# Performance work log

Hardware: AMD Instinct MI355X
Metric: run time of the kernel (lower is better)

## Reference

```python
import jax, jax.numpy as jnp
import numpy as np

NUM_HEADS = 4
HID = 64
NUM_LAYERS = 3
NEG_SLOPE = 0.2  # PyG GATConv default


def setup_inputs() -> dict:
    key = jax.random.key(0)
    ks = jax.random.split(key, 6)
    B, N, D = 64, 512, 64
    return {
        "embeddings": jax.random.normal(ks[0], (B, N, D), jnp.float32),
        "lin_w": jax.random.normal(ks[1], (NUM_LAYERS, NUM_HEADS * HID, D), jnp.float32) * 0.1,
        "att_src": jax.random.normal(ks[2], (NUM_LAYERS, NUM_HEADS, HID), jnp.float32) * 0.1,
        "att_dst": jax.random.normal(ks[3], (NUM_LAYERS, NUM_HEADS, HID), jnp.float32) * 0.1,
        "conv_b": jnp.zeros((NUM_LAYERS, HID), jnp.float32),
        "readout_w": jax.random.normal(ks[4], (D, HID), jnp.float32) * 0.1,
        "readout_b": jnp.zeros((D,), jnp.float32),
    }


def reference(embeddings, lin_w, att_src, att_dst, conv_b, readout_w, readout_b):
    # Graph is fully connected (combinations + reversed) and PyG GATConv adds
    # self-loops by default -> attention softmax over ALL nodes j for each i.
    B, N, _ = embeddings.shape
    x = embeddings
    for l in range(NUM_LAYERS):
        h = jnp.einsum('bnd,od->bno', x, lin_w[l]).reshape(B, N, NUM_HEADS, HID)  # [B,N,H,C]
        a_src = jnp.einsum('bnhc,hc->bnh', h, att_src[l])  # per source node j
        a_dst = jnp.einsum('bnhc,hc->bnh', h, att_dst[l])  # per target node i
        e = a_dst[:, :, None, :] + a_src[:, None, :, :]    # [B,i,j,H]
        e = jnp.where(e >= 0, e, NEG_SLOPE * e)            # LeakyReLU(0.2)
        alpha = jax.nn.softmax(e, axis=2)                  # softmax over neighbors j
        out = jnp.einsum('bijh,bjhc->bihc', alpha, h).mean(axis=2) + conv_b[l]  # concat=False -> head mean
        x = jax.nn.relu(out)
    pooled = x.mean(axis=1)                                # mean over nodes
    return pooled @ readout_w.T + readout_b                # [B, D]
```

## Files before the change

### kernel.cpp

```cpp
#include <hip/hip_runtime.h>
#include <math.h>


using short8  = __attribute__((ext_vector_type(8))) short;
using floatx4 = __attribute__((ext_vector_type(4))) float;

__device__ inline unsigned short f2bf(float f) {
    union { float f; unsigned u; } v; v.f = f;
    unsigned u = v.u + 0x7FFFu + ((v.u >> 16) & 1u);
    return (unsigned short)(u >> 16);
}
__device__ inline float bf2f(unsigned short s) {
    union { float f; unsigned u; } v; v.u = ((unsigned)s) << 16;
    return v.f;
}

__device__ inline void cvt8(const float4 a, const float4 b, short8& hi, short8& lo) {
    float f[8] = {a.x, a.y, a.z, a.w, b.x, b.y, b.z, b.w};
    short8 H, L;
#pragma unroll
    for (int i = 0; i < 8; ++i) {
        unsigned short h = f2bf(f[i]);
        H[i] = (short)h;
        L[i] = (short)f2bf(f[i] - bf2f(h));
    }
    hi = H; lo = L;
}

__global__ __launch_bounds__(512) void linprep_kernel(const float* __restrict__ x,
                                                      const float* __restrict__ W,
                                                      const float* __restrict__ att_src,
                                                      const float* __restrict__ att_dst,
                                                      float* __restrict__ hT,
                                                      float4* __restrict__ g_rE,
                                                      float4* __restrict__ g_abk) {
    __shared__ unsigned short WH[64 * 72], WL[64 * 72];
    __shared__ float sA[512], dA[512];
    __shared__ int   s_idxE[512];
    __shared__ float z1suf[513], z2pre[513];
    __shared__ float wred[8];

    const int t  = threadIdx.x;
    const int r8 = blockIdx.x & 7;
    const int q  = blockIdx.x >> 3;
    const int ct = q & 3;
    const int b  = ((q >> 2) << 3) | r8;
    const int bh = b * 4 + ct;
    const int c0 = ct * 64;

#pragma unroll
    for (int qq = 0; qq < 2; ++qq) {
        int f = qq * 512 + t;
        int wrow = f >> 4, d4 = f & 15;
        float4 v = *(const float4*)(W + (size_t)(c0 + wrow) * 64 + d4 * 4);
        unsigned short h0 = f2bf(v.x), h1 = f2bf(v.y), h2 = f2bf(v.z), h3 = f2bf(v.w);
        ushort4 hi = make_ushort4(h0, h1, h2, h3);
        ushort4 lo = make_ushort4(f2bf(v.x - bf2f(h0)), f2bf(v.y - bf2f(h1)),
                                  f2bf(v.z - bf2f(h2)), f2bf(v.w - bf2f(h3)));
        *(ushort4*)&WH[wrow * 72 + d4 * 4] = hi;
        *(ushort4*)&WL[wrow * 72 + d4 * 4] = lo;
    }
    __syncthreads();

    const int lane = t & 63, wv = t >> 6;
    const int mrow = lane & 15, quad = lane >> 4;

    short8 bhf[4][2], blf[4][2];
#pragma unroll
    for (int g = 0; g < 4; ++g)
#pragma unroll
        for (int kk = 0; kk < 2; ++kk) {
            int ko = kk * 32 + quad * 8;
            bhf[g][kk] = *(const short8*)&WH[(g * 16 + mrow) * 72 + ko];
            blf[g][kk] = *(const short8*)&WL[(g * 16 + mrow) * 72 + ko];
        }
    float as_g[4], ad_g[4];
#pragma unroll
    for (int g = 0; g < 4; ++g) {
        as_g[g] = att_src[c0 + g * 16 + mrow];
        ad_g[g] = att_dst[c0 + g * 16 + mrow];
    }

    const float* xbase = x + (size_t)(b * 512 + mrow) * 64 + quad * 8;
    float4 nxa = *(const float4*)(xbase + (size_t)wv * 1024);
    float4 nxb = *(const float4*)(xbase + (size_t)wv * 1024 + 4);
    float4 nxc = *(const float4*)(xbase + (size_t)wv * 1024 + 32);
    float4 nxd = *(const float4*)(xbase + (size_t)wv * 1024 + 36);

#pragma unroll 1
    for (int tl = wv; tl < 32; tl += 8) {
        float4 xa = nxa, xb = nxb, xc = nxc, xd = nxd;
        if (tl + 8 < 32) {
            const float* nb = xbase + (size_t)(tl + 8) * 1024;
            nxa = *(const float4*)(nb);
            nxb = *(const float4*)(nb + 4);
            nxc = *(const float4*)(nb + 32);
            nxd = *(const float4*)(nb + 36);
        }
        short8 ah0, al0, ah1, al1;
        cvt8(xa, xb, ah0, al0);
        cvt8(xc, xd, ah1, al1);

        floatx4 acc[4];
#pragma unroll
        for (int g = 0; g < 4; ++g) {
            floatx4 a = {0.f, 0.f, 0.f, 0.f};
            a = __builtin_amdgcn_mfma_f32_16x16x32_bf16(ah0, bhf[g][0], a, 0, 0, 0);
            a = __builtin_amdgcn_mfma_f32_16x16x32_bf16(ah1, bhf[g][1], a, 0, 0, 0);
            a = __builtin_amdgcn_mfma_f32_16x16x32_bf16(ah0, blf[g][0], a, 0, 0, 0);
            a = __builtin_amdgcn_mfma_f32_16x16x32_bf16(ah1, blf[g][1], a, 0, 0, 0);
            a = __builtin_amdgcn_mfma_f32_16x16x32_bf16(al0, bhf[g][0], a, 0, 0, 0);
            a = __builtin_amdgcn_mfma_f32_16x16x32_bf16(al1, bhf[g][1], a, 0, 0, 0);
            acc[g] = a;
        }

        const int nbase = b * 512 + tl * 16 + quad * 4;
#pragma unroll
        for (int g = 0; g < 4; ++g) {
            float tmp0 = __shfl_xor(acc[g][0], 1, 64);
            float tmp1 = __shfl_xor(acc[g][1], 1, 64);
            float tmp2 = __shfl_xor(acc[g][2], 1, 64);
            float tmp3 = __shfl_xor(acc[g][3], 1, 64);
            const size_t cp = (size_t)(ct * 32 + g * 8 + (mrow >> 1));
            if ((mrow & 1) == 0) {
                *(float4*)&hT[cp * 65536 + (size_t)nbase * 2] =
                    make_float4(acc[g][0], tmp0, acc[g][1], tmp1);
            } else {
                *(float4*)&hT[cp * 65536 + (size_t)(nbase + 2) * 2] =
                    make_float4(tmp2, acc[g][2], tmp3, acc[g][3]);
            }
        }

        float ps[4], pd[4];
#pragma unroll
        for (int reg = 0; reg < 4; ++reg) {
            ps[reg] = acc[0][reg] * as_g[0] + acc[1][reg] * as_g[1]
                    + acc[2][reg] * as_g[2] + acc[3][reg] * as_g[3];
            pd[reg] = acc[0][reg] * ad_g[0] + acc[1][reg] * ad_g[1]
                    + acc[2][reg] * ad_g[2] + acc[3][reg] * ad_g[3];
        }
#pragma unroll
        for (int m = 1; m <= 8; m <<= 1) {
#pragma unroll
            for (int reg = 0; reg < 4; ++reg) {
                ps[reg] += __shfl_xor(ps[reg], m, 64);
                pd[reg] += __shfl_xor(pd[reg], m, 64);
            }
        }
        if (mrow < 4) {
            sA[tl * 16 + quad * 4 + mrow] = ps[mrow];
            dA[tl * 16 + quad * 4 + mrow] = pd[mrow];
        }
    }
    __syncthreads();

    const bool act = (t < 256);
    const int wid = t >> 6;

    float dreg[2] = {0.f, 0.f};
    if (act) {
        dreg[0] = dA[t];
        dreg[1] = dA[t + 256];
    }

    float v0 = 0.f, v1 = 0.f;
    int id0 = 0, id1 = 0;
    if (act) { v0 = sA[2 * t]; v1 = sA[2 * t + 1]; id0 = 2 * t; id1 = 2 * t + 1; }

    for (int k = 2; k <= 512; k <<= 1) {
        for (int j = k >> 1; j >= 1; j >>= 1) {
            bool asc = ((t & (k >> 1)) == 0);
            if (j == 1) {
                if (act) {
                    bool sw = asc ? (v0 > v1) : (v0 < v1);
                    if (sw) { float tv = v0; v0 = v1; v1 = tv; int ti = id0; id0 = id1; id1 = ti; }
                }
            } else if (j <= 64) {
                if (act) {
                    int m = j >> 1;
                    float w0 = __shfl_xor(v0, m, 64);
                    int  wi0 = __shfl_xor(id0, m, 64);
                    float w1 = __shfl_xor(v1, m, 64);
                    int  wi1 = __shfl_xor(id1, m, 64);
                    bool low = ((t & m) == 0);
                    bool wantmin = (low == asc);
                    if (wantmin ? (w0 < v0) : (w0 > v0)) { v0 = w0; id0 = wi0; }
                    if (wantmin ? (w1 < v1) : (w1 > v1)) { v1 = w1; id1 = wi1; }
                }
            } else {
                int m = j >> 1;
                if (act) {
                    sA[2 * t] = v0; sA[2 * t + 1] = v1;
                    s_idxE[2 * t] = id0; s_idxE[2 * t + 1] = id1;
                }
                __syncthreads();
                if (act) {
                    int tp = t ^ m;
                    float w0 = sA[2 * tp], w1 = sA[2 * tp + 1];
                    int wi0 = s_idxE[2 * tp], wi1 = s_idxE[2 * tp + 1];
                    bool low = ((t & m) == 0);
                    bool wantmin = (low == asc);
                    if (wantmin ? (w0 < v0) : (w0 > v0)) { v0 = w0; id0 = wi0; }
                    if (wantmin ? (w1 < v1) : (w1 > v1)) { v1 = w1; id1 = wi1; }
                }
                __syncthreads();
            }
        }
    }

    if (act) { sA[2 * t] = v0; sA[2 * t + 1] = v1; }
    __syncthreads();
    const float M = sA[511];

    float e1_0 = 0.f, e1_1 = 0.f, e2_0 = 0.f, e2_1 = 0.f;
    if (act) {
        e1_0 = __expf(v0 - M);  e1_1 = __expf(v1 - M);
        e2_0 = __expf(0.2f * (v0 - M));  e2_1 = __expf(0.2f * (v1 - M));
        const int base = bh * 512;
        g_rE[base + id0] = make_float4(__int_as_float(2 * t),     e1_0, e2_0, 0.f);
        g_rE[base + id1] = make_float4(__int_as_float(2 * t + 1), e1_1, e2_1, 0.f);
    }

    float S1 = e1_0 + e1_1, S2 = e2_0 + e2_1;
    float i1 = S1, i2 = S2;
    if (act) {
        for (int off = 1; off < 64; off <<= 1) {
            float u1 = __shfl_up(i1, off, 64);
            float u2 = __shfl_up(i2, off, 64);
            if (lane >= off) { i1 += u1; i2 += u2; }
        }
        if (lane == 63) { wred[wid] = i1; wred[4 + wid] = i2; }
    }
    __syncthreads();
    if (act) {
        float off1 = 0.f, off2 = 0.f;
        for (int w = 0; w < wid; ++w) { off1 += wred[w]; off2 += wred[4 + w]; }
        const float T1 = wred[0] + wred[1] + wred[2] + wred[3];
        const float T2 = wred[4] + wred[5] + wred[6] + wred[7];
        float pre1 = off1 + i1 - S1;
        float pre2 = off2 + i2 - S2;
        z1suf[2 * t] = T1 - pre1;
        z1suf[2 * t + 1] = T1 - pre1 - e1_0;
        z2pre[2 * t] = pre2;
        z2pre[2 * t + 1] = pre2 + e2_0;
        if (t == 0) { z1suf[512] = 0.f; z2pre[512] = T2; }
    }
    __syncthreads();

    if (act) {
        for (int rr = 0; rr < 2; ++rr) {
            int i = t + rr * 256;
            float d = dreg[rr];
            int lo = 0, hi = 512;
            while (lo < hi) {
                int mid = (lo + hi) >> 1;
                if (d + sA[mid] >= 0.f) hi = mid; else lo = mid + 1;
            }
            int k = lo;
            float g = d + M;
            float G = (g >= 0.f) ? g : 0.2f * g;
            float al = __expf(g - G);
            float be = __expf(0.2f * g - G);
            float Z = al * z1suf[k] + be * z2pre[k];
            float inv = 1.0f / Z;
            g_abk[bh * 512 + i] = make_float4(al * inv, be * inv,
                                              __int_as_float(k), 0.f);
        }
    }
}

__global__ __launch_bounds__(256) void attn_agg_fin(const float* __restrict__ hT,
                                                    const float4* __restrict__ g_rE,
                                                    const float4* __restrict__ g_abk,
                                                    const float* __restrict__ bias,
                                                    float* __restrict__ x,
                                                    float* __restrict__ pooled,
                                                    int storex) {
    const int r8 = blockIdx.x & 7;
    const int qq = blockIdx.x >> 3;
    const int cg = qq & 31;
    const int b  = ((qq >> 5) << 3) | r8;
    const int c0 = cg * 2;
    const int t = threadIdx.x;
    const int lane = t & 63, wv = t >> 6;

    __shared__ float4 A12[4][512];
    __shared__ float tots[4][2];
    __shared__ float sredP[4][2];

    {
        const int bh = b * 4 + wv;
        const int base = bh * 512;
        const float* hTb = hT + (size_t)(wv * 32 + cg) * 65536 + (size_t)(b * 512) * 2;
#pragma unroll
        for (int it = 0; it < 8; ++it) {
            int j = it * 64 + lane;
            float4 rE = g_rE[base + j];
            int rk = __float_as_int(rE.x);
            float2 hv = *(const float2*)&hTb[j * 2];
            int pk = ((rk & 7) << 6) | (rk >> 3);
            A12[wv][pk] = make_float4(rE.y * hv.x, rE.z * hv.x,
                                      rE.y * hv.y, rE.z * hv.y);
        }
        float a1c0[8], a2c0[8], a1c1[8], a2c1[8];
#pragma unroll
        for (int i = 0; i < 8; ++i) {
            float4 vv = A12[wv][i * 64 + lane];
            a1c0[i] = vv.x; a2c0[i] = vv.y; a1c1[i] = vv.z; a2c1[i] = vv.w;
        }
        float s10 = 0.f, s20 = 0.f, s11 = 0.f, s21 = 0.f;
#pragma unroll
        for (int i = 0; i < 8; ++i) {
            s10 += a1c0[i]; s20 += a2c0[i]; s11 += a1c1[i]; s21 += a2c1[i];
        }
        float suf0 = s10, suf1 = s11;
#pragma unroll
        for (int off = 1; off < 64; off <<= 1) {
            float u0 = __shfl_down(suf0, off, 64);
            float u1 = __shfl_down(suf1, off, 64);
            if (lane + off < 64) { suf0 += u0; suf1 += u1; }
        }
        float run0 = suf0 - s10, run1 = suf1 - s11;
        float pre0 = s20, pre1 = s21;
#pragma unroll
        for (int off = 1; off < 64; off <<= 1) {
            float u0 = __shfl_up(pre0, off, 64);
            float u1 = __shfl_up(pre1, off, 64);
            if (lane >= off) { pre0 += u0; pre1 += u1; }
        }
        float run20 = pre0 - s20, run21 = pre1 - s21;
        if (lane == 63) { tots[wv][0] = pre0; tots[wv][1] = pre1; }
#pragma unroll
        for (int i = 7; i >= 0; --i) {
            run0 += a1c0[i]; a1c0[i] = run0;
            run1 += a1c1[i]; a1c1[i] = run1;
        }
#pragma unroll
        for (int i = 0; i < 8; ++i) {
            float tv0 = a2c0[i]; a2c0[i] = run20; run20 += tv0;
            float tv1 = a2c1[i]; a2c1[i] = run21; run21 += tv1;
        }
#pragma unroll
        for (int i = 0; i < 8; ++i)
            A12[wv][i * 64 + lane] = make_float4(a1c0[i], a2c0[i],
                                                 a1c1[i], a2c1[i]);
    }
    __syncthreads();

    const float bv0 = bias[c0], bv1 = bias[c0 + 1];
    float p0 = 0.f, p1 = 0.f;
#pragma unroll
    for (int rr = 0; rr < 2; ++rr) {
        const int i = t + rr * 256;
        float a0 = 0.f, a1 = 0.f;
#pragma unroll
        for (int head = 0; head < 4; ++head) {
            const int base = (b * 4 + head) * 512;
            float4 abk = g_abk[base + i];
            int k = __float_as_int(abk.z);
            if (k < 512) {
                int pk = ((k & 7) << 6) | (k >> 3);
                float4 vv = A12[head][pk];
                a0 += abk.x * vv.x + abk.y * vv.y;
                a1 += abk.x * vv.z + abk.y * vv.w;
            } else {
                a0 += abk.y * tots[head][0];
                a1 += abk.y * tots[head][1];
            }
        }
        float2 o = make_float2(fmaxf(0.25f * a0 + bv0, 0.f),
                               fmaxf(0.25f * a1 + bv1, 0.f));
        if (storex) *(float2*)&x[(size_t)(b * 512 + i) * 64 + c0] = o;
        p0 += o.x; p1 += o.y;
    }

#pragma unroll
    for (int m = 1; m <= 32; m <<= 1) {
        p0 += __shfl_xor(p0, m, 64);
        p1 += __shfl_xor(p1, m, 64);
    }
    if (lane == 0) { sredP[wv][0] = p0; sredP[wv][1] = p1; }
    __syncthreads();
    if (t == 0) {
        pooled[b * 64 + c0]     = sredP[0][0] + sredP[1][0] + sredP[2][0] + sredP[3][0];
        pooled[b * 64 + c0 + 1] = sredP[0][1] + sredP[1][1] + sredP[2][1] + sredP[3][1];
    }
}

__global__ __launch_bounds__(64) void readout_kernel(const float* __restrict__ pooled,
                                                     const float* __restrict__ rw,
                                                     const float* __restrict__ rb,
                                                     float* __restrict__ out) {
    __shared__ float pl[64];
    int b = blockIdx.x, t = threadIdx.x;
    pl[t] = pooled[b * 64 + t] * (1.0f / 512.0f);
    __syncthreads();
    float a = rb[t];
    for (int cc = 0; cc < 64; ++cc) a += pl[cc] * rw[t * 64 + cc];
    out[b * 64 + t] = a;
}

extern "C" void kernel_launch(void* const* d_in, const int* in_sizes, int n_in,
                              void* d_out, int out_size, void* d_ws, size_t ws_size,
                              hipStream_t stream) {
    const float* emb       = (const float*)d_in[0];
    const float* lin_w     = (const float*)d_in[1];
    const float* att_src   = (const float*)d_in[2];
    const float* att_dst   = (const float*)d_in[3];
    const float* conv_b    = (const float*)d_in[4];
    const float* readout_w = (const float*)d_in[5];
    const float* readout_b = (const float*)d_in[6];
    float* out = (float*)d_out;

    float* ws   = (float*)d_ws;
    float* xbuf = ws;
    float* hT   = ws + 2097152;
    float* meta = ws + 10485760;

    float4* g_rE   = (float4*)meta;
    float4* g_abk  = (float4*)(meta + 524288);
    float*  pooled = ws + 11534336;

    for (int l = 0; l < 3; ++l) {
        const float* xin = (l == 0) ? emb : xbuf;
        linprep_kernel<<<256, 512, 0, stream>>>(xin, lin_w + (size_t)l * 16384,
                                                att_src + l * 256, att_dst + l * 256,
                                                hT, g_rE, g_abk);
        attn_agg_fin<<<2048, 256, 0, stream>>>(hT, g_rE, g_abk,
                                               conv_b + l * 64, xbuf, pooled,
                                               (l < 2) ? 1 : 0);
    }
    readout_kernel<<<64, 64, 0, stream>>>(pooled, readout_w, readout_b, out);
}
```

Baseline: 196.4 us.

## Split fused linear+prep kernel into parallel GEMM and separate sort/prefix kernel

The fused linprep kernel ran 256 blocks of 512 threads, with half the threads idle during the sort and prefix phase. This splits it into a lin_kernel over 1024 blocks of 256 threads, where each block handles a quarter of the node tiles and writes src/dst attention scores to a global buffer. A new prep_kernel with 256 blocks of 256 threads then does the bitonic sort, prefix sums and per-row search. The aim is more parallelism and occupancy for the GEMM; the cost is an extra launch per layer, a global round-trip for the scores, and re-converting the weight tile to bf16 in four times as many blocks.

```diff
diff --git a/kernel.cpp b/kernel.cpp
--- a/kernel.cpp
+++ b/kernel.cpp
@@ -27,30 +27,27 @@
     hi = H; lo = L;
 }
 
-__global__ __launch_bounds__(512) void linprep_kernel(const float* __restrict__ x,
-                                                      const float* __restrict__ W,
-                                                      const float* __restrict__ att_src,
-                                                      const float* __restrict__ att_dst,
-                                                      float* __restrict__ hT,
-                                                      float4* __restrict__ g_rE,
-                                                      float4* __restrict__ g_abk) {
+__global__ __launch_bounds__(256) void lin_kernel(const float* __restrict__ x,
+                                                  const float* __restrict__ W,
+                                                  const float* __restrict__ att_src,
+                                                  const float* __restrict__ att_dst,
+                                                  float* __restrict__ hT,
+                                                  float2* __restrict__ g_sd) {
     __shared__ unsigned short WH[64 * 72], WL[64 * 72];
-    __shared__ float sA[512], dA[512];
-    __shared__ int   s_idxE[512];
-    __shared__ float z1suf[513], z2pre[513];
-    __shared__ float wred[8];
 
     const int t  = threadIdx.x;
-    const int r8 = blockIdx.x & 7;
-    const int q  = blockIdx.x >> 3;
-    const int ct = q & 3;
-    const int b  = ((q >> 2) << 3) | r8;
-    const int bh = b * 4 + ct;
-    const int c0 = ct * 64;
-
-#pragma unroll
-    for (int qq = 0; qq < 2; ++qq) {
-        int f = qq * 512 + t;
+    const int r8   = blockIdx.x & 7;
+    const int rest = blockIdx.x >> 3;
+    const int bhi  = rest >> 4;
+    const int ct   = (rest >> 2) & 3;
+    const int q4   = rest & 3;
+    const int b    = (bhi << 3) | r8;
+    const int bh   = b * 4 + ct;
+    const int c0   = ct * 64;
+
+#pragma unroll
+    for (int qq = 0; qq < 4; ++qq) {
+        int f = qq * 256 + t;
         int wrow = f >> 4, d4 = f & 15;
         float4 v = *(const float4*)(W + (size_t)(c0 + wrow) * 64 + d4 * 4);
         unsigned short h0 = f2bf(v.x), h1 = f2bf(v.y), h2 = f2bf(v.z), h3 = f2bf(v.w);
@@ -81,17 +78,19 @@
         ad_g[g] = att_dst[c0 + g * 16 + mrow];
     }
 
+    const int tl0 = q4 * 8 + wv;
     const float* xbase = x + (size_t)(b * 512 + mrow) * 64 + quad * 8;
-    float4 nxa = *(const float4*)(xbase + (size_t)wv * 1024);
-    float4 nxb = *(const float4*)(xbase + (size_t)wv * 1024 + 4);
-    float4 nxc = *(const float4*)(xbase + (size_t)wv * 1024 + 32);
-    float4 nxd = *(const float4*)(xbase + (size_t)wv * 1024 + 36);
+    float4 nxa = *(const float4*)(xbase + (size_t)tl0 * 1024);
+    float4 nxb = *(const float4*)(xbase + (size_t)tl0 * 1024 + 4);
+    float4 nxc = *(const float4*)(xbase + (size_t)tl0 * 1024 + 32);
+    float4 nxd = *(const float4*)(xbase + (size_t)tl0 * 1024 + 36);
 
 #pragma unroll 1
-    for (int tl = wv; tl < 32; tl += 8) {
+    for (int ii = 0; ii < 2; ++ii) {
+        const int tl = tl0 + ii * 4;
         float4 xa = nxa, xb = nxb, xc = nxc, xd = nxd;
-        if (tl + 8 < 32) {
-            const float* nb = xbase + (size_t)(tl + 8) * 1024;
+        if (ii == 0) {
+            const float* nb = xbase + (size_t)(tl + 4) * 1024;
             nxa = *(const float4*)(nb);
             nxb = *(const float4*)(nb + 4);
             nxc = *(const float4*)(nb + 32);
@@ -148,74 +147,76 @@
             }
         }
         if (mrow < 4) {
-            sA[tl * 16 + quad * 4 + mrow] = ps[mrow];
-            dA[tl * 16 + quad * 4 + mrow] = pd[mrow];
-        }
-    }
-    __syncthreads();
-
-    const bool act = (t < 256);
+            g_sd[bh * 512 + tl * 16 + quad * 4 + mrow] =
+                make_float2(ps[mrow], pd[mrow]);
+        }
+    }
+}
+
+__global__ __launch_bounds__(256) void prep_kernel(const float2* __restrict__ g_sd,
+                                                   float4* __restrict__ g_rE,
+                                                   float4* __restrict__ g_abk) {
+    __shared__ float sA[512], dA[512];
+    __shared__ int   s_idxE[512];
+    __shared__ float z1suf[513], z2pre[513];
+    __shared__ float wred[8];
+
+    const int bh = blockIdx.x;
+    const int t = threadIdx.x;
+    const int lane = t & 63;
     const int wid = t >> 6;
 
-    float dreg[2] = {0.f, 0.f};
-    if (act) {
-        dreg[0] = dA[t];
-        dreg[1] = dA[t + 256];
-    }
-
-    float v0 = 0.f, v1 = 0.f;
-    int id0 = 0, id1 = 0;
-    if (act) { v0 = sA[2 * t]; v1 = sA[2 * t + 1]; id0 = 2 * t; id1 = 2 * t + 1; }
-
+    for (int rr = 0; rr < 2; ++rr) {
+        int j = t + rr * 256;
+        float2 sd = g_sd[bh * 512 + j];
+        sA[j] = sd.x;
+        dA[j] = sd.y;
+    }
+    __syncthreads();
+
+    float dreg[2] = {dA[t], dA[t + 256]};
+
+    float v0 = sA[2 * t], v1 = sA[2 * t + 1];
+    int id0 = 2 * t, id1 = 2 * t + 1;
     for (int k = 2; k <= 512; k <<= 1) {
         for (int j = k >> 1; j >= 1; j >>= 1) {
             bool asc = ((t & (k >> 1)) == 0);
             if (j == 1) {
-                if (act) {
-                    bool sw = asc ? (v0 > v1) : (v0 < v1);
-                    if (sw) { float tv = v0; v0 = v1; v1 = tv; int ti = id0; id0 = id1; id1 = ti; }
-                }
+                bool sw = asc ? (v0 > v1) : (v0 < v1);
+                if (sw) { float tv = v0; v0 = v1; v1 = tv; int ti = id0; id0 = id1; id1 = ti; }
             } else if (j <= 64) {
-                if (act) {
-                    int m = j >> 1;
-                    float w0 = __shfl_xor(v0, m, 64);
-                    int  wi0 = __shfl_xor(id0, m, 64);
-                    float w1 = __shfl_xor(v1, m, 64);
-                    int  wi1 = __shfl_xor(id1, m, 64);
-                    bool low = ((t & m) == 0);
-                    bool wantmin = (low == asc);
-                    if (wantmin ? (w0 < v0) : (w0 > v0)) { v0 = w0; id0 = wi0; }
-                    if (wantmin ? (w1 < v1) : (w1 > v1)) { v1 = w1; id1 = wi1; }
-                }
+                int m = j >> 1;
+                float w0 = __shfl_xor(v0, m, 64);
+                int  wi0 = __shfl_xor(id0, m, 64);
+                float w1 = __shfl_xor(v1, m, 64);
+                int  wi1 = __shfl_xor(id1, m, 64);
+                bool low = ((t & m) == 0);
+                bool wantmin = (low == asc);
+                if (wantmin ? (w0 < v0) : (w0 > v0)) { v0 = w0; id0 = wi0; }
+                if (wantmin ? (w1 < v1) : (w1 > v1)) { v1 = w1; id1 = wi1; }
             } else {
                 int m = j >> 1;
-                if (act) {
-                    sA[2 * t] = v0; sA[2 * t + 1] = v1;
-                    s_idxE[2 * t] = id0; s_idxE[2 * t + 1] = id1;
-                }
+                sA[2 * t] = v0; sA[2 * t + 1] = v1;
+                s_idxE[2 * t] = id0; s_idxE[2 * t + 1] = id1;
                 __syncthreads();
-                if (act) {
-                    int tp = t ^ m;
-                    float w0 = sA[2 * tp], w1 = sA[2 * tp + 1];
-                    int wi0 = s_idxE[2 * tp], wi1 = s_idxE[2 * tp + 1];
-                    bool low = ((t & m) == 0);
-                    bool wantmin = (low == asc);
-                    if (wantmin ? (w0 < v0) : (w0 > v0)) { v0 = w0; id0 = wi0; }
-                    if (wantmin ? (w1 < v1) : (w1 > v1)) { v1 = w1; id1 = wi1; }
-                }
+                int tp = t ^ m;
+                float w0 = sA[2 * tp], w1 = sA[2 * tp + 1];
+                int wi0 = s_idxE[2 * tp], wi1 = s_idxE[2 * tp + 1];
+                bool low = ((t & m) == 0);
+                bool wantmin = (low == asc);
+                if (wantmin ? (w0 < v0) : (w0 > v0)) { v0 = w0; id0 = wi0; }
+                if (wantmin ? (w1 < v1) : (w1 > v1)) { v1 = w1; id1 = wi1; }
                 __syncthreads();
             }
         }
     }
 
-    if (act) { sA[2 * t] = v0; sA[2 * t + 1] = v1; }
+    sA[2 * t] = v0; sA[2 * t + 1] = v1;
     __syncthreads();
     const float M = sA[511];
-
-    float e1_0 = 0.f, e1_1 = 0.f, e2_0 = 0.f, e2_1 = 0.f;
-    if (act) {
-        e1_0 = __expf(v0 - M);  e1_1 = __expf(v1 - M);
-        e2_0 = __expf(0.2f * (v0 - M));  e2_1 = __expf(0.2f * (v1 - M));
+    float e1_0 = __expf(v0 - M), e1_1 = __expf(v1 - M);
+    float e2_0 = __expf(0.2f * (v0 - M)), e2_1 = __expf(0.2f * (v1 - M));
+    {
         const int base = bh * 512;
         g_rE[base + id0] = make_float4(__int_as_float(2 * t),     e1_0, e2_0, 0.f);
         g_rE[base + id1] = make_float4(__int_as_float(2 * t + 1), e1_1, e2_1, 0.f);
@@ -223,49 +224,43 @@
 
     float S1 = e1_0 + e1_1, S2 = e2_0 + e2_1;
     float i1 = S1, i2 = S2;
-    if (act) {
-        for (int off = 1; off < 64; off <<= 1) {
-            float u1 = __shfl_up(i1, off, 64);
-            float u2 = __shfl_up(i2, off, 64);
-            if (lane >= off) { i1 += u1; i2 += u2; }
-        }
-        if (lane == 63) { wred[wid] = i1; wred[4 + wid] = i2; }
-    }
-    __syncthreads();
-    if (act) {
-        float off1 = 0.f, off2 = 0.f;
-        for (int w = 0; w < wid; ++w) { off1 += wred[w]; off2 += wred[4 + w]; }
-        const float T1 = wred[0] + wred[1] + wred[2] + wred[3];
-        const float T2 = wred[4] + wred[5] + wred[6] + wred[7];
-        float pre1 = off1 + i1 - S1;
-        float pre2 = off2 + i2 - S2;
-        z1suf[2 * t] = T1 - pre1;
-        z1suf[2 * t + 1] = T1 - pre1 - e1_0;
-        z2pre[2 * t] = pre2;
-        z2pre[2 * t + 1] = pre2 + e2_0;
-        if (t == 0) { z1suf[512] = 0.f; z2pre[512] = T2; }
-    }
-    __syncthreads();
-
-    if (act) {
-        for (int rr = 0; rr < 2; ++rr) {
-            int i = t + rr * 256;
-            float d = dreg[rr];
-            int lo = 0, hi = 512;
-            while (lo < hi) {
-                int mid = (lo + hi) >> 1;
-                if (d + sA[mid] >= 0.f) hi = mid; else lo = mid + 1;
-            }
-            int k = lo;
-            float g = d + M;
-            float G = (g >= 0.f) ? g : 0.2f * g;
-            float al = __expf(g - G);
-            float be = __expf(0.2f * g - G);
-            float Z = al * z1suf[k] + be * z2pre[k];
-            float inv = 1.0f / Z;
-            g_abk[bh * 512 + i] = make_float4(al * inv, be * inv,
-                                              __int_as_float(k), 0.f);
-        }
+    for (int off = 1; off < 64; off <<= 1) {
+        float u1 = __shfl_up(i1, off, 64);
+        float u2 = __shfl_up(i2, off, 64);
+        if (lane >= off) { i1 += u1; i2 += u2; }
+    }
+    if (lane == 63) { wred[wid] = i1; wred[4 + wid] = i2; }
+    __syncthreads();
+    float off1 = 0.f, off2 = 0.f;
+    for (int w = 0; w < wid; ++w) { off1 += wred[w]; off2 += wred[4 + w]; }
+    const float T1 = wred[0] + wred[1] + wred[2] + wred[3];
+    const float T2 = wred[4] + wred[5] + wred[6] + wred[7];
+    float pre1 = off1 + i1 - S1;
+    float pre2 = off2 + i2 - S2;
+    z1suf[2 * t] = T1 - pre1;
+    z1suf[2 * t + 1] = T1 - pre1 - e1_0;
+    z2pre[2 * t] = pre2;
+    z2pre[2 * t + 1] = pre2 + e2_0;
+    if (t == 0) { z1suf[512] = 0.f; z2pre[512] = T2; }
+    __syncthreads();
+
+    for (int rr = 0; rr < 2; ++rr) {
+        int i = t + rr * 256;
+        float d = dreg[rr];
+        int lo = 0, hi = 512;
+        while (lo < hi) {
+            int mid = (lo + hi) >> 1;
+            if (d + sA[mid] >= 0.f) hi = mid; else lo = mid + 1;
+        }
+        int k = lo;
+        float g = d + M;
+        float G = (g >= 0.f) ? g : 0.2f * g;
+        float al = __expf(g - G);
+        float be = __expf(0.2f * g - G);
+        float Z = al * z1suf[k] + be * z2pre[k];
+        float inv = 1.0f / Z;
+        g_abk[bh * 512 + i] = make_float4(al * inv, be * inv,
+                                          __int_as_float(k), 0.f);
     }
 }
 
@@ -420,12 +415,14 @@
     float4* g_rE   = (float4*)meta;
     float4* g_abk  = (float4*)(meta + 524288);
     float*  pooled = ws + 11534336;
+    float2* g_sd   = (float2*)(ws + 11538432);
 
     for (int l = 0; l < 3; ++l) {
         const float* xin = (l == 0) ? emb : xbuf;
-        linprep_kernel<<<256, 512, 0, stream>>>(xin, lin_w + (size_t)l * 16384,
-                                                att_src + l * 256, att_dst + l * 256,
-                                                hT, g_rE, g_abk);
+        lin_kernel<<<1024, 256, 0, stream>>>(xin, lin_w + (size_t)l * 16384,
+                                             att_src + l * 256, att_dst + l * 256,
+                                             hT, g_sd);
+        prep_kernel<<<256, 256, 0, stream>>>(g_sd, g_rE, g_abk);
         attn_agg_fin<<<2048, 256, 0, stream>>>(hT, g_rE, g_abk,
                                                conv_b + l * 64, xbuf, pooled,
                                                (l < 2) ? 1 : 0);
```

Result: slower. 205.8 us (+4.8%).
